# Kernel optimization log

Hardware: AMD Instinct MI355X
Metric: run time of the kernel (lower is better)

The kernel has to match this reference:

```python
import jax, jax.numpy as jnp
import numpy as np

B, T_OUT, L, D, H = 1, 8, 512, 512, 8  # batch, frames, tokens/frame, d_model, heads


def setup_inputs() -> dict:
    key = jax.random.key(0)
    ks = jax.random.split(key, 7)
    return {
        "hidden_states": jax.random.normal(ks[0], (B * T_OUT, L, D), jnp.float32),
        "p_out": jax.random.normal(ks[1], (B, T_OUT, 4, 4), jnp.float32),
        "p_out_inv": jax.random.normal(ks[2], (B, T_OUT, 4, 4), jnp.float32),
        "Wq": jax.random.normal(ks[3], (D, D), jnp.float32) * 0.02,
        "Wk": jax.random.normal(ks[4], (D, D), jnp.float32) * 0.02,
        "Wv": jax.random.normal(ks[5], (D, D), jnp.float32) * 0.02,
        "Wo": jax.random.normal(ks[6], (D, D), jnp.float32) * 0.02,
        "bo": jnp.zeros((D,), jnp.float32),
        "num_heads": H,
    }


def cape_embed(f, P):
    # f: (b, S, d), P: (b, S, 4, 4); rearrange '(d k)'->'d k' with k=4, matmul by P, flatten back
    b, S, d = f.shape
    f4 = f.reshape(b, S, d // 4, 4)
    return jnp.einsum('bsdk,bskg->bsdg', f4, P).reshape(b, S, d)


def reference(hidden_states, p_out, p_out_inv, Wq, Wk, Wv, Wo, bo, num_heads):
    b, t_out = p_out.shape[0], p_out.shape[1]
    bt, l, d = hidden_states.shape
    S = t_out * l
    residual = hidden_states

    # '(b t_out) l d -> b (t_out l) d'
    x = hidden_states.reshape(b, S, d)

    q = x @ Wq
    k = x @ Wk
    v = x @ Wv

    # repeat per-frame CAPE matrices over tokens within each frame; self-attn so p_in = p_out
    Pq = jnp.repeat(p_out_inv, l, axis=1)  # (b, S, 4, 4)
    Pk = jnp.repeat(p_out, l, axis=1)      # (b, S, 4, 4)
    q = cape_embed(q, Pq)
    k = cape_embed(k, Pk)

    hd = d // num_heads
    scale = hd ** -0.5
    qh = q.reshape(b, S, num_heads, hd).transpose(0, 2, 1, 3)  # (b, h, S, hd)
    kh = k.reshape(b, S, num_heads, hd).transpose(0, 2, 1, 3)
    vh = v.reshape(b, S, num_heads, hd).transpose(0, 2, 1, 3)

    scores = jnp.einsum('bhqd,bhkd->bhqk', qh, kh) * scale  # full (b,h,S,S) matrix
    probs = jax.nn.softmax(scores, axis=-1)
    o = jnp.einsum('bhqk,bhkd->bhqd', probs, vh)

    o = o.transpose(0, 2, 1, 3).reshape(b, S, d)
    o = o @ Wo + bo  # to_out[0]; to_out[1] dropout is identity in eval

    # 'b (t_out l) d -> (b t_out) l d'
    o = o.reshape(bt, l, d)
    return o + residual  # residual_connection; rescale_output_factor = 1.0
```

## Files before the change

### kernel.cpp

```cpp
#include <hip/hip_runtime.h>
#include <hip/hip_bf16.h>
#include <stdint.h>

typedef __bf16 bf16_t;
typedef __bf16 bf16x2 __attribute__((ext_vector_type(2)));
typedef __bf16 bf16x4 __attribute__((ext_vector_type(4)));
typedef __bf16 bf16x8 __attribute__((ext_vector_type(8)));
typedef float f32x4 __attribute__((ext_vector_type(4)));

#define MFMA(a, b, c) __builtin_amdgcn_mfma_f32_16x16x32_bf16(a, b, c, 0, 0, 0)

#if __has_builtin(__builtin_amdgcn_exp2f)
#define FEXP2 __builtin_amdgcn_exp2f
#else
#define FEXP2 exp2f
#endif

__device__ __forceinline__ void g2lds16(const void* g, void* l) {
  __builtin_amdgcn_global_load_lds(
      reinterpret_cast<const __attribute__((address_space(1))) unsigned int*>(
          reinterpret_cast<uintptr_t>(g)),
      reinterpret_cast<__attribute__((address_space(3))) unsigned int*>(
          reinterpret_cast<uintptr_t>(l)),
      16, 0, 0);
}

__global__ __launch_bounds__(256) void k_cvt_x(const float* __restrict__ x,
                                               bf16_t* __restrict__ y) {
  int i = (blockIdx.x * 256 + threadIdx.x) * 4;
  float4 v = *reinterpret_cast<const float4*>(x + i);
  bf16x4 o;
  o[0] = (bf16_t)v.x; o[1] = (bf16_t)v.y; o[2] = (bf16_t)v.z; o[3] = (bf16_t)v.w;
  *reinterpret_cast<bf16x4*>(y + i) = o;
}

__global__ __launch_bounds__(256) void k_prep_qk(const float* __restrict__ Wq,
                                                 const float* __restrict__ Wk,
                                                 const float* __restrict__ Pout,
                                                 const float* __restrict__ Pinv,
                                                 bf16_t* __restrict__ WqT,
                                                 bf16_t* __restrict__ WkT) {
  int idx = blockIdx.x * 256 + threadIdx.x;
  int t = idx >> 15;
  int n = (idx >> 6) & 511;
  int k0 = (idx & 63) << 3;
  int dq4 = (n >> 2) << 2;
  int g = n & 3;
  float pq[4], pk[4];
#pragma unroll
  for (int h = 0; h < 4; ++h) {
    pq[h] = Pinv[t * 16 + h * 4 + g];
    pk[h] = Pout[t * 16 + h * 4 + g];
  }
  bf16x8 oq, ok;
#pragma unroll
  for (int j = 0; j < 8; ++j) {
    const float4 wq = *reinterpret_cast<const float4*>(Wq + (size_t)(k0 + j) * 512 + dq4);
    const float4 wk = *reinterpret_cast<const float4*>(Wk + (size_t)(k0 + j) * 512 + dq4);
    oq[j] = (bf16_t)((wq.x * pq[0] + wq.y * pq[1] + wq.z * pq[2] + wq.w * pq[3]) * 0.1803368801f);
    ok[j] = (bf16_t)(wk.x * pk[0] + wk.y * pk[1] + wk.z * pk[2] + wk.w * pk[3]);
  }
  size_t o = ((size_t)t * 512 + n) * 512 + k0;
  *reinterpret_cast<bf16x8*>(WqT + o) = oq;
  *reinterpret_cast<bf16x8*>(WkT + o) = ok;
}

__global__ __launch_bounds__(256) void k_prep_vo(const float* __restrict__ Wv,
                                                 const float* __restrict__ Wo,
                                                 bf16_t* __restrict__ WvT,
                                                 bf16_t* __restrict__ WoT) {
  int idx = blockIdx.x * 256 + threadIdx.x;
  int mat = idx >> 15;
  int n = (idx >> 6) & 511;
  int k0 = (idx & 63) << 3;
  const float* W = mat ? Wo : Wv;
  bf16_t* T = mat ? WoT : WvT;
  bf16x8 o;
#pragma unroll
  for (int j = 0; j < 8; ++j) o[j] = (bf16_t)W[(size_t)(k0 + j) * 512 + n];
  *reinterpret_cast<bf16x8*>(T + (size_t)n * 512 + k0) = o;
}

__global__ __launch_bounds__(256) void k_gemm_qkv(const bf16_t* __restrict__ Xbf,
                                                  const bf16_t* __restrict__ WqT,
                                                  const bf16_t* __restrict__ WkT,
                                                  const bf16_t* __restrict__ WvT,
                                                  bf16_t* __restrict__ Qh,
                                                  bf16_t* __restrict__ Kh,
                                                  bf16_t* __restrict__ Vt) {
  __shared__ bf16_t lA[128 * 64];
  __shared__ bf16_t lB[64 * 64];
  const int m0 = blockIdx.x * 128, n0 = blockIdx.y * 64;
  const int mat = blockIdx.z;
  const int frame = m0 >> 9;
  const bf16_t* WT = (mat == 0) ? (WqT + (size_t)frame * 512 * 512)
                   : (mat == 1) ? (WkT + (size_t)frame * 512 * 512)
                                : WvT;
  const int tid = threadIdx.x, lane = tid & 63, wid = tid >> 6;
  const int wr = wid >> 1, wc = wid & 1;
  const int l15 = lane & 15, lg = lane >> 4;
  const int srow = lane >> 3;
  const int scol = ((lane & 7) ^ (lane >> 3)) << 3;

  f32x4 acc[4][2] = {};

  for (int kt = 0; kt < 512; kt += 64) {
#pragma unroll
    for (int i = 0; i < 4; ++i) {
      int chunk = wid * 4 + i;
      int row = chunk * 8 + srow;
      g2lds16(Xbf + (size_t)(m0 + row) * 512 + kt + scol, lA + chunk * 512);
    }
#pragma unroll
    for (int i = 0; i < 2; ++i) {
      int chunk = wid * 2 + i;
      int row = chunk * 8 + srow;
      g2lds16(WT + (size_t)(n0 + row) * 512 + kt + scol, lB + chunk * 512);
    }
    __syncthreads();
#pragma unroll
    for (int kk = 0; kk < 2; ++kk) {
      bf16x8 af[4], bw[2];
      int c16 = ((4 * kk + lg) ^ (l15 & 7)) << 3;
#pragma unroll
      for (int i = 0; i < 4; ++i)
        af[i] = *reinterpret_cast<const bf16x8*>(lA + (wr * 64 + i * 16 + l15) * 64 + c16);
#pragma unroll
      for (int j = 0; j < 2; ++j)
        bw[j] = *reinterpret_cast<const bf16x8*>(lB + (wc * 32 + j * 16 + l15) * 64 + c16);
#pragma unroll
      for (int i = 0; i < 4; ++i)
#pragma unroll
        for (int j = 0; j < 2; ++j)
          acc[i][j] = MFMA(af[i], bw[j], acc[i][j]);
    }
    __syncthreads();
  }

#pragma unroll
  for (int i = 0; i < 4; ++i)
#pragma unroll
    for (int j = 0; j < 2; ++j)
#pragma unroll
      for (int r = 0; r < 4; ++r) {
        int s = m0 + wr * 64 + i * 16 + lg * 4 + r;
        int n = n0 + wc * 32 + j * 16 + l15;
        bf16_t v = (bf16_t)acc[i][j][r];
        if (mat == 2) {
          Vt[(size_t)n * 4096 + s] = v;
        } else if (mat == 0) {
          Qh[((size_t)(n >> 6) * 4096 + s) * 64 + (n & 63)] = v;
        } else {
          Kh[((size_t)(n >> 6) * 4096 + s) * 64 + (n & 63)] = v;
        }
      }
}

__global__ __launch_bounds__(256, 4) void k_attn(const bf16_t* __restrict__ Qh,
                                                 const bf16_t* __restrict__ Kh,
                                                 const bf16_t* __restrict__ Vt,
                                                 char* __restrict__ wsb,
                                                 float* __restrict__ Mp,
                                                 float* __restrict__ Lp) {
  __shared__ bf16_t lK[2][64 * 64];
  __shared__ bf16_t lV[2][64 * 64];
  __shared__ bf16_t lP[4 * 16 * 64];
  const int h = blockIdx.y;
  const int ks = blockIdx.z;
  const int q0 = blockIdx.x * 128;
  const int tid = threadIdx.x, lane = tid & 63, wid = tid >> 6;
  const int l15 = lane & 15, lg = lane >> 4;
  const int srow = lane >> 3;
  const int scol = ((lane & 7) ^ (lane >> 3)) << 3;

  bf16_t* Op = (bf16_t*)(ks < 3 ? wsb + ((size_t)ks << 22) : wsb + (29u << 20));

  bf16x8 qf[2][2];
#pragma unroll
  for (int g = 0; g < 2; ++g) {
    const bf16_t* Qp = Qh + ((size_t)h * 4096 + q0 + wid * 32 + g * 16 + l15) * 64;
#pragma unroll
    for (int kk = 0; kk < 2; ++kk)
      qf[g][kk] = *reinterpret_cast<const bf16x8*>(Qp + kk * 32 + lg * 8);
  }

  bf16x8 onesf;
#pragma unroll
  for (int j = 0; j < 8; ++j) onesf[j] = (bf16_t)1.0f;

  const bf16_t* Kb = Kh + ((size_t)h * 4096 + ks * 1024) * 64;
  const bf16_t* Vb = Vt + (size_t)h * 64 * 4096 + ks * 1024;

  f32x4 oT[2][4] = {};
  f32x4 lac[2] = {};
  float m[2] = {-3e38f, -3e38f};
  bf16_t* Pw = lP + wid * 1024;

  auto stage = [&](int buf, int kt) {
#pragma unroll
    for (int i = 0; i < 2; ++i) {
      int chunk = wid * 2 + i;
      int row = chunk * 8 + srow;
      g2lds16(Kb + (size_t)(kt + row) * 64 + scol, &lK[buf][chunk * 512]);
      g2lds16(Vb + (size_t)row * 4096 + kt + scol, &lV[buf][chunk * 512]);
    }
  };

  stage(0, 0);
  __syncthreads();

  for (int t = 0; t < 16; ++t) {
    const int cur = t & 1;
    if (t < 15) stage(cur ^ 1, (t + 1) * 64);

    f32x4 st[2][4] = {};
    __builtin_amdgcn_s_setprio(1);
#pragma unroll
    for (int kk = 0; kk < 2; ++kk)
#pragma unroll
      for (int mb = 0; mb < 4; ++mb) {
        bf16x8 kf = *reinterpret_cast<const bf16x8*>(
            &lK[cur][(mb * 16 + l15) * 64 + (((kk * 4 + lg) ^ (l15 & 7)) << 3)]);
        st[0][mb] = MFMA(kf, qf[0][kk], st[0][mb]);
        st[1][mb] = MFMA(kf, qf[1][kk], st[1][mb]);
      }
    __builtin_amdgcn_s_setprio(0);

#pragma unroll
    for (int g = 0; g < 2; ++g) {
      float t0 = fmaxf(fmaxf(st[g][0][0], st[g][0][1]), fmaxf(st[g][0][2], st[g][0][3]));
      float t1 = fmaxf(fmaxf(st[g][1][0], st[g][1][1]), fmaxf(st[g][1][2], st[g][1][3]));
      float t2 = fmaxf(fmaxf(st[g][2][0], st[g][2][1]), fmaxf(st[g][2][2], st[g][2][3]));
      float t3 = fmaxf(fmaxf(st[g][3][0], st[g][3][1]), fmaxf(st[g][3][2], st[g][3][3]));
      float tmax = fmaxf(fmaxf(t0, t1), fmaxf(t2, t3));
      tmax = fmaxf(tmax, __shfl_xor(tmax, 16, 64));
      tmax = fmaxf(tmax, __shfl_xor(tmax, 32, 64));
      if (!__all(tmax <= m[g] + 8.f)) {
        float mnew = fmaxf(m[g], tmax);
        float corr = FEXP2(m[g] - mnew);
        m[g] = mnew;
        lac[g] *= corr;
#pragma unroll
        for (int hb = 0; hb < 4; ++hb) oT[g][hb] *= corr;
      }
#pragma unroll
      for (int mb = 0; mb < 4; ++mb)
#pragma unroll
        for (int r = 0; r < 4; ++r)
          st[g][mb][r] = FEXP2(st[g][mb][r] - m[g]);
    }

    bf16x8 pb[2][2];
#pragma unroll
    for (int g = 0; g < 2; ++g) {
#pragma unroll
      for (int mb = 0; mb < 4; ++mb) {
        int key0 = mb * 16 + lg * 4;
        int c16 = (key0 >> 3) ^ (l15 & 7);
        bf16_t* p = Pw + l15 * 64 + c16 * 8 + (key0 & 7);
        bf16x2 p01, p23;
        p01[0] = (bf16_t)st[g][mb][0]; p01[1] = (bf16_t)st[g][mb][1];
        p23[0] = (bf16_t)st[g][mb][2]; p23[1] = (bf16_t)st[g][mb][3];
        *reinterpret_cast<bf16x2*>(p) = p01;
        *reinterpret_cast<bf16x2*>(p + 2) = p23;
      }
#pragma unroll
      for (int kk = 0; kk < 2; ++kk)
        pb[g][kk] = *reinterpret_cast<const bf16x8*>(
            Pw + l15 * 64 + (((kk * 4 + lg) ^ (l15 & 7)) << 3));
    }

    __builtin_amdgcn_s_setprio(1);
#pragma unroll
    for (int kk = 0; kk < 2; ++kk) {
      lac[0] = MFMA(onesf, pb[0][kk], lac[0]);
      lac[1] = MFMA(onesf, pb[1][kk], lac[1]);
#pragma unroll
      for (int hb = 0; hb < 4; ++hb) {
        bf16x8 vf = *reinterpret_cast<const bf16x8*>(
            &lV[cur][(hb * 16 + l15) * 64 + (((kk * 4 + lg) ^ (l15 & 7)) << 3)]);
        oT[0][hb] = MFMA(vf, pb[0][kk], oT[0][hb]);
        oT[1][hb] = MFMA(vf, pb[1][kk], oT[1][hb]);
      }
    }
    __builtin_amdgcn_s_setprio(0);
    __syncthreads();
  }

#pragma unroll
  for (int g = 0; g < 2; ++g) {
    int q = q0 + wid * 32 + g * 16 + l15;
    size_t rbase = ((size_t)ks * 8 + h) * 4096 + q;
    size_t obase = ((size_t)h * 4096 + q) * 64;
    if (lg == 0) { Mp[rbase] = m[g]; Lp[rbase] = lac[g][0]; }
#pragma unroll
    for (int hb = 0; hb < 4; ++hb) {
      bf16x4 ov;
#pragma unroll
      for (int r = 0; r < 4; ++r) ov[r] = (bf16_t)oT[g][hb][r];
      *reinterpret_cast<bf16x4*>(Op + obase + hb * 16 + lg * 4) = ov;
    }
  }
}

__global__ __launch_bounds__(256) void k_merge(char* __restrict__ wsb,
                                               const float* __restrict__ Mp,
                                               const float* __restrict__ Lp,
                                               bf16_t* __restrict__ Obf) {
  int idx = blockIdx.x * 256 + threadIdx.x;
  int d4 = (idx & 15) << 2;
  int row = idx >> 4;
  float ms[4];
  float mstar = -3e38f;
#pragma unroll
  for (int s = 0; s < 4; ++s) {
    ms[s] = Mp[s * 32768 + row];
    mstar = fmaxf(mstar, ms[s]);
  }
  float l = 0.f;
  f32x4 o = {};
#pragma unroll
  for (int s = 0; s < 4; ++s) {
    const bf16_t* Ops = (const bf16_t*)(s < 3 ? wsb + ((size_t)s << 22) : wsb + (29u << 20));
    float w = FEXP2(ms[s] - mstar);
    l += w * Lp[s * 32768 + row];
    bf16x4 v = *reinterpret_cast<const bf16x4*>(Ops + (size_t)row * 64 + d4);
    o[0] += w * (float)v[0]; o[1] += w * (float)v[1];
    o[2] += w * (float)v[2]; o[3] += w * (float)v[3];
  }
  float rinv = 1.f / l;
  int h = row >> 12, q = row & 4095;
  bf16x4 ov;
#pragma unroll
  for (int r = 0; r < 4; ++r) ov[r] = (bf16_t)(o[r] * rinv);
  *reinterpret_cast<bf16x4*>(Obf + (size_t)q * 512 + h * 64 + d4) = ov;
}

__global__ __launch_bounds__(256) void k_gemm_out(const bf16_t* __restrict__ Obf,
                                                  const bf16_t* __restrict__ WoT,
                                                  const float* __restrict__ bo,
                                                  const float* __restrict__ resid,
                                                  float* __restrict__ out) {
  __shared__ bf16_t lA[64 * 64];
  __shared__ bf16_t lB[64 * 64];
  const int m0 = blockIdx.x * 64, n0 = blockIdx.y * 64;
  const int tid = threadIdx.x, lane = tid & 63, wid = tid >> 6;
  const int wr = wid >> 1, wc = wid & 1;
  const int l15 = lane & 15, lg = lane >> 4;
  const int srow = lane >> 3;
  const int scol = ((lane & 7) ^ (lane >> 3)) << 3;

  f32x4 acc[2][2] = {};

  for (int kt = 0; kt < 512; kt += 64) {
#pragma unroll
    for (int i = 0; i < 2; ++i) {
      int chunk = wid * 2 + i;
      int row = chunk * 8 + srow;
      g2lds16(Obf + (size_t)(m0 + row) * 512 + kt + scol, lA + chunk * 512);
      g2lds16(WoT + (size_t)(n0 + row) * 512 + kt + scol, lB + chunk * 512);
    }
    __syncthreads();
#pragma unroll
    for (int kk = 0; kk < 2; ++kk) {
      bf16x8 af[2], bw[2];
      int c16 = ((4 * kk + lg) ^ (l15 & 7)) << 3;
#pragma unroll
      for (int i = 0; i < 2; ++i) {
        af[i] = *reinterpret_cast<const bf16x8*>(lA + (wr * 32 + i * 16 + l15) * 64 + c16);
        bw[i] = *reinterpret_cast<const bf16x8*>(lB + (wc * 32 + i * 16 + l15) * 64 + c16);
      }
#pragma unroll
      for (int i = 0; i < 2; ++i)
#pragma unroll
        for (int j = 0; j < 2; ++j)
          acc[i][j] = MFMA(af[i], bw[j], acc[i][j]);
    }
    __syncthreads();
  }

#pragma unroll
  for (int i = 0; i < 2; ++i)
#pragma unroll
    for (int j = 0; j < 2; ++j)
#pragma unroll
      for (int r = 0; r < 4; ++r) {
        int s = m0 + wr * 32 + i * 16 + lg * 4 + r;
        int n = n0 + wc * 32 + j * 16 + l15;
        size_t o = (size_t)s * 512 + n;
        out[o] = acc[i][j][r] + bo[n] + resid[o];
      }
}

extern "C" void kernel_launch(void* const* d_in, const int* in_sizes, int n_in,
                              void* d_out, int out_size, void* d_ws, size_t ws_size,
                              hipStream_t stream) {
  const float* hs   = (const float*)d_in[0];
  const float* pout = (const float*)d_in[1];
  const float* pinv = (const float*)d_in[2];
  const float* Wq   = (const float*)d_in[3];
  const float* Wk   = (const float*)d_in[4];
  const float* Wv   = (const float*)d_in[5];
  const float* Wo   = (const float*)d_in[6];
  const float* bo   = (const float*)d_in[7];
  float* out = (float*)d_out;

  char* ws = (char*)d_ws;
  bf16_t* Xbf = (bf16_t*)(ws);
  bf16_t* WqT = (bf16_t*)(ws + (4u << 20));
  bf16_t* WkT = (bf16_t*)(ws + (8u << 20));
  bf16_t* WvT = (bf16_t*)(ws + (12u << 20));
  bf16_t* WoT = (bf16_t*)(ws + (12u << 20) + (512u << 10));
  bf16_t* Qh  = (bf16_t*)(ws + (13u << 20));
  bf16_t* Kh  = (bf16_t*)(ws + (17u << 20));
  bf16_t* Vt  = (bf16_t*)(ws + (21u << 20));
  bf16_t* Obf = (bf16_t*)(ws + (25u << 20));
  float*  Mp  = (float*)(ws + (33u << 20));
  float*  Lp  = (float*)(ws + (33u << 20) + (512u << 10));

  hipLaunchKernelGGL(k_cvt_x, dim3(2048), dim3(256), 0, stream, hs, Xbf);
  hipLaunchKernelGGL(k_prep_qk, dim3(1024), dim3(256), 0, stream, Wq, Wk, pout, pinv, WqT, WkT);
  hipLaunchKernelGGL(k_prep_vo, dim3(256), dim3(256), 0, stream, Wv, Wo, WvT, WoT);
  hipLaunchKernelGGL(k_gemm_qkv, dim3(32, 8, 3), dim3(256), 0, stream,
                     Xbf, WqT, WkT, WvT, Qh, Kh, Vt);
  hipLaunchKernelGGL(k_attn, dim3(32, 8, 4), dim3(256), 0, stream, Qh, Kh, Vt, ws, Mp, Lp);
  hipLaunchKernelGGL(k_merge, dim3(2048), dim3(256), 0, stream, ws, Mp, Lp, Obf);
  hipLaunchKernelGGL(k_gemm_out, dim3(64, 8), dim3(256), 0, stream, Obf, WoT, bo, hs, out);
}
```

Measured before the change: 115.4 us.

## Merge prep kernels into one launch and single-buffer attention K/V tiles

Combines the three preprocessing kernels (x conversion, Q/K weight folding with CAPE, V/O transpose) into one launch that dispatches work by block index, saving two kernel launches. In the attention kernel, K/V staging moves from double-buffered prefetch to a single LDS buffer loaded at the top of each iteration and followed by a barrier. This halves K/V LDS use, which may allow more resident blocks. In exchange it drops the overlap of the next tile's global loads with current compute, exposing load latency each iteration.

```diff
diff --git a/kernel.cpp b/kernel.cpp
--- a/kernel.cpp
+++ b/kernel.cpp
@@ -25,60 +25,61 @@
       16, 0, 0);
 }
 
-__global__ __launch_bounds__(256) void k_cvt_x(const float* __restrict__ x,
-                                               bf16_t* __restrict__ y) {
-  int i = (blockIdx.x * 256 + threadIdx.x) * 4;
-  float4 v = *reinterpret_cast<const float4*>(x + i);
-  bf16x4 o;
-  o[0] = (bf16_t)v.x; o[1] = (bf16_t)v.y; o[2] = (bf16_t)v.z; o[3] = (bf16_t)v.w;
-  *reinterpret_cast<bf16x4*>(y + i) = o;
-}
-
-__global__ __launch_bounds__(256) void k_prep_qk(const float* __restrict__ Wq,
-                                                 const float* __restrict__ Wk,
-                                                 const float* __restrict__ Pout,
-                                                 const float* __restrict__ Pinv,
-                                                 bf16_t* __restrict__ WqT,
-                                                 bf16_t* __restrict__ WkT) {
-  int idx = blockIdx.x * 256 + threadIdx.x;
-  int t = idx >> 15;
-  int n = (idx >> 6) & 511;
-  int k0 = (idx & 63) << 3;
-  int dq4 = (n >> 2) << 2;
-  int g = n & 3;
-  float pq[4], pk[4];
-#pragma unroll
-  for (int h = 0; h < 4; ++h) {
-    pq[h] = Pinv[t * 16 + h * 4 + g];
-    pk[h] = Pout[t * 16 + h * 4 + g];
-  }
-  bf16x8 oq, ok;
-#pragma unroll
-  for (int j = 0; j < 8; ++j) {
-    const float4 wq = *reinterpret_cast<const float4*>(Wq + (size_t)(k0 + j) * 512 + dq4);
-    const float4 wk = *reinterpret_cast<const float4*>(Wk + (size_t)(k0 + j) * 512 + dq4);
-    oq[j] = (bf16_t)((wq.x * pq[0] + wq.y * pq[1] + wq.z * pq[2] + wq.w * pq[3]) * 0.1803368801f);
-    ok[j] = (bf16_t)(wk.x * pk[0] + wk.y * pk[1] + wk.z * pk[2] + wk.w * pk[3]);
-  }
-  size_t o = ((size_t)t * 512 + n) * 512 + k0;
-  *reinterpret_cast<bf16x8*>(WqT + o) = oq;
-  *reinterpret_cast<bf16x8*>(WkT + o) = ok;
-}
-
-__global__ __launch_bounds__(256) void k_prep_vo(const float* __restrict__ Wv,
-                                                 const float* __restrict__ Wo,
-                                                 bf16_t* __restrict__ WvT,
-                                                 bf16_t* __restrict__ WoT) {
-  int idx = blockIdx.x * 256 + threadIdx.x;
-  int mat = idx >> 15;
-  int n = (idx >> 6) & 511;
-  int k0 = (idx & 63) << 3;
-  const float* W = mat ? Wo : Wv;
-  bf16_t* T = mat ? WoT : WvT;
-  bf16x8 o;
-#pragma unroll
-  for (int j = 0; j < 8; ++j) o[j] = (bf16_t)W[(size_t)(k0 + j) * 512 + n];
-  *reinterpret_cast<bf16x8*>(T + (size_t)n * 512 + k0) = o;
+__global__ __launch_bounds__(256) void k_prep(const float* __restrict__ x,
+                                              const float* __restrict__ Wq,
+                                              const float* __restrict__ Wk,
+                                              const float* __restrict__ Wv,
+                                              const float* __restrict__ Wo,
+                                              const float* __restrict__ Pout,
+                                              const float* __restrict__ Pinv,
+                                              bf16_t* __restrict__ Xbf,
+                                              bf16_t* __restrict__ WqT,
+                                              bf16_t* __restrict__ WkT,
+                                              bf16_t* __restrict__ WvT,
+                                              bf16_t* __restrict__ WoT) {
+  const int bid = blockIdx.x;
+  if (bid < 2048) {
+    int i = (bid * 256 + threadIdx.x) * 4;
+    float4 v = *reinterpret_cast<const float4*>(x + i);
+    bf16x4 o;
+    o[0] = (bf16_t)v.x; o[1] = (bf16_t)v.y; o[2] = (bf16_t)v.z; o[3] = (bf16_t)v.w;
+    *reinterpret_cast<bf16x4*>(Xbf + i) = o;
+  } else if (bid < 3072) {
+    int idx = (bid - 2048) * 256 + threadIdx.x;
+    int t = idx >> 15;
+    int n = (idx >> 6) & 511;
+    int k0 = (idx & 63) << 3;
+    int dq4 = (n >> 2) << 2;
+    int g = n & 3;
+    float pq[4], pk[4];
+#pragma unroll
+    for (int h = 0; h < 4; ++h) {
+      pq[h] = Pinv[t * 16 + h * 4 + g];
+      pk[h] = Pout[t * 16 + h * 4 + g];
+    }
+    bf16x8 oq, ok;
+#pragma unroll
+    for (int j = 0; j < 8; ++j) {
+      const float4 wq = *reinterpret_cast<const float4*>(Wq + (size_t)(k0 + j) * 512 + dq4);
+      const float4 wk = *reinterpret_cast<const float4*>(Wk + (size_t)(k0 + j) * 512 + dq4);
+      oq[j] = (bf16_t)((wq.x * pq[0] + wq.y * pq[1] + wq.z * pq[2] + wq.w * pq[3]) * 0.1803368801f);
+      ok[j] = (bf16_t)(wk.x * pk[0] + wk.y * pk[1] + wk.z * pk[2] + wk.w * pk[3]);
+    }
+    size_t o = ((size_t)t * 512 + n) * 512 + k0;
+    *reinterpret_cast<bf16x8*>(WqT + o) = oq;
+    *reinterpret_cast<bf16x8*>(WkT + o) = ok;
+  } else {
+    int idx = (bid - 3072) * 256 + threadIdx.x;
+    int mat = idx >> 15;
+    int n = (idx >> 6) & 511;
+    int k0 = (idx & 63) << 3;
+    const float* W = mat ? Wo : Wv;
+    bf16_t* T = mat ? WoT : WvT;
+    bf16x8 o;
+#pragma unroll
+    for (int j = 0; j < 8; ++j) o[j] = (bf16_t)W[(size_t)(k0 + j) * 512 + n];
+    *reinterpret_cast<bf16x8*>(T + (size_t)n * 512 + k0) = o;
+  }
 }
 
 __global__ __launch_bounds__(256) void k_gemm_qkv(const bf16_t* __restrict__ Xbf,
@@ -162,8 +163,8 @@
                                                  char* __restrict__ wsb,
                                                  float* __restrict__ Mp,
                                                  float* __restrict__ Lp) {
-  __shared__ bf16_t lK[2][64 * 64];
-  __shared__ bf16_t lV[2][64 * 64];
+  __shared__ bf16_t lK[64 * 64];
+  __shared__ bf16_t lV[64 * 64];
   __shared__ bf16_t lP[4 * 16 * 64];
   const int h = blockIdx.y;
   const int ks = blockIdx.z;
@@ -196,22 +197,15 @@
   float m[2] = {-3e38f, -3e38f};
   bf16_t* Pw = lP + wid * 1024;
 
-  auto stage = [&](int buf, int kt) {
+  for (int t = 0; t < 16; ++t) {
 #pragma unroll
     for (int i = 0; i < 2; ++i) {
       int chunk = wid * 2 + i;
       int row = chunk * 8 + srow;
-      g2lds16(Kb + (size_t)(kt + row) * 64 + scol, &lK[buf][chunk * 512]);
-      g2lds16(Vb + (size_t)row * 4096 + kt + scol, &lV[buf][chunk * 512]);
-    }
-  };
-
-  stage(0, 0);
-  __syncthreads();
-
-  for (int t = 0; t < 16; ++t) {
-    const int cur = t & 1;
-    if (t < 15) stage(cur ^ 1, (t + 1) * 64);
+      g2lds16(Kb + (size_t)(t * 64 + row) * 64 + scol, lK + chunk * 512);
+      g2lds16(Vb + (size_t)row * 4096 + t * 64 + scol, lV + chunk * 512);
+    }
+    __syncthreads();
 
     f32x4 st[2][4] = {};
     __builtin_amdgcn_s_setprio(1);
@@ -220,7 +214,7 @@
 #pragma unroll
       for (int mb = 0; mb < 4; ++mb) {
         bf16x8 kf = *reinterpret_cast<const bf16x8*>(
-            &lK[cur][(mb * 16 + l15) * 64 + (((kk * 4 + lg) ^ (l15 & 7)) << 3)]);
+            lK + (mb * 16 + l15) * 64 + (((kk * 4 + lg) ^ (l15 & 7)) << 3));
         st[0][mb] = MFMA(kf, qf[0][kk], st[0][mb]);
         st[1][mb] = MFMA(kf, qf[1][kk], st[1][mb]);
       }
@@ -278,7 +272,7 @@
 #pragma unroll
       for (int hb = 0; hb < 4; ++hb) {
         bf16x8 vf = *reinterpret_cast<const bf16x8*>(
-            &lV[cur][(hb * 16 + l15) * 64 + (((kk * 4 + lg) ^ (l15 & 7)) << 3)]);
+            lV + (hb * 16 + l15) * 64 + (((kk * 4 + lg) ^ (l15 & 7)) << 3));
         oT[0][hb] = MFMA(vf, pb[0][kk], oT[0][hb]);
         oT[1][hb] = MFMA(vf, pb[1][kk], oT[1][hb]);
       }
@@ -418,9 +412,8 @@
   float*  Mp  = (float*)(ws + (33u << 20));
   float*  Lp  = (float*)(ws + (33u << 20) + (512u << 10));
 
-  hipLaunchKernelGGL(k_cvt_x, dim3(2048), dim3(256), 0, stream, hs, Xbf);
-  hipLaunchKernelGGL(k_prep_qk, dim3(1024), dim3(256), 0, stream, Wq, Wk, pout, pinv, WqT, WkT);
-  hipLaunchKernelGGL(k_prep_vo, dim3(256), dim3(256), 0, stream, Wv, Wo, WvT, WoT);
+  hipLaunchKernelGGL(k_prep, dim3(3328), dim3(256), 0, stream,
+                     hs, Wq, Wk, Wv, Wo, pout, pinv, Xbf, WqT, WkT, WvT, WoT);
   hipLaunchKernelGGL(k_gemm_qkv, dim3(32, 8, 3), dim3(256), 0, stream,
                      Xbf, WqT, WkT, WvT, Qh, Kh, Vt);
   hipLaunchKernelGGL(k_attn, dim3(32, 8, 4), dim3(256), 0, stream, Qh, Kh, Vt, ws, Mp, Lp);
```

Result: faster. 107.9 us (-6.5%).
